# Kernel tuning notes

Measured on AMD Instinct MI355X. Metric: run time of the kernel, lower is better.

## Reference

```python
import jax, jax.numpy as jnp
import numpy as np

IN_DIM = 2048
OUT_DIM = 2048
BASIS_DIM = 64
BATCH = 4
SEQ = 4096
EPS = 1e-5


def _make_bbasis():
    k = np.arange(BASIS_DIM, dtype=np.float64)[:, None]  # (K,1)
    i = np.arange(OUT_DIM, dtype=np.float64)[None, :]    # (1,D)
    return jnp.asarray(np.cos(2.0 * np.pi * (k + 1.0) / (i + 2.0)), dtype=jnp.float32)


def setup_inputs() -> dict:
    key = jax.random.key(0)
    k1, k2, k3, k4 = jax.random.split(key, 4)
    x = jax.random.normal(k1, (BATCH, SEQ, IN_DIM), dtype=jnp.float32)
    # nn.init.uniform_(-0.1, 0.1) style scaling for weights
    W = jax.random.uniform(k2, (OUT_DIM, IN_DIM), dtype=jnp.float32, minval=-0.1, maxval=0.1)
    W_res = jax.random.uniform(k3, (OUT_DIM, IN_DIM), dtype=jnp.float32, minval=-0.1, maxval=0.1)
    Acoeff = jax.random.uniform(k4, (OUT_DIM, BASIS_DIM), dtype=jnp.float32, minval=-0.1, maxval=0.1)
    gamma = jnp.ones((OUT_DIM,), dtype=jnp.float32)
    beta = jnp.zeros((OUT_DIM,), dtype=jnp.float32)
    Bbasis = _make_bbasis()
    return {"x": x, "W": W, "W_res": W_res, "gamma": gamma, "beta": beta,
            "Acoeff": Acoeff, "Bbasis": Bbasis}


def reference(x, W, W_res, gamma, beta, Acoeff, Bbasis):
    # residual projection (use_residual == 'separate')
    residual = jnp.einsum('bsi,oi->bso', x, W_res)          # (B,S,D)
    transformed = jnp.einsum('bsi,oi->bso', x, W)           # (B,S,D)
    # LayerNorm over last dim
    mean = jnp.mean(transformed, axis=-1, keepdims=True)
    var = jnp.mean(jnp.square(transformed - mean), axis=-1, keepdims=True)
    normalized = (transformed - mean) * jax.lax.rsqrt(var + EPS) * gamma + beta
    # periodic basis gather
    seq_len = x.shape[1]
    j = jnp.arange(seq_len) % BASIS_DIM                      # (S,)
    B_vec = Bbasis[j]                                        # (S,D)
    A_vec = Acoeff[:, j].T                                   # (S,D)
    scalars = jnp.einsum('bsd,sd->bs', normalized, B_vec)    # (B,S)
    return scalars[:, :, None] * A_vec[None] + residual      # (B,S,D)
```

## Files before the change

kernel.cpp:

```cpp
#include <hip/hip_runtime.h>
#include <hip/hip_bf16.h>

#define KDIM   2048
#define DDIM   2048
#define MROWS  16384
#define BASIS  64
#define EPSLN  1e-5f

typedef __bf16 bf16x8 __attribute__((ext_vector_type(8)));
typedef float  f32x4  __attribute__((ext_vector_type(4)));

static __device__ __forceinline__ unsigned short f2bf(float f) {
  union { float f; unsigned int u; } v; v.f = f;
  unsigned int r = v.u + 0x7FFFu + ((v.u >> 16) & 1u);
  return (unsigned short)(r >> 16);
}

__global__ __launch_bounds__(256) void cast_f32_bf16(
    const float* __restrict__ in, unsigned short* __restrict__ out, int n4) {
  int i = blockIdx.x * blockDim.x + threadIdx.x;
  int stride = gridDim.x * blockDim.x;
  for (; i < n4; i += stride) {
    float4 v = ((const float4*)in)[i];
    ushort4 o;
    o.x = f2bf(v.x); o.y = f2bf(v.y); o.z = f2bf(v.z); o.w = f2bf(v.w);
    ((ushort4*)out)[i] = o;
  }
}

__global__ __launch_bounds__(256) void transpose_acoeff(
    const float* __restrict__ Ac, float* __restrict__ At) {
  int j = blockIdx.x;
  for (int d = threadIdx.x; d < DDIM; d += blockDim.x)
    At[j * DDIM + d] = Ac[d * BASIS + j];
}

__device__ __forceinline__ void gload16(const void* g, void* l) {
  __builtin_amdgcn_global_load_lds(
      (const __attribute__((address_space(1))) unsigned int*)(unsigned long long)g,
      (__attribute__((address_space(3))) unsigned int*)(unsigned int)(unsigned long long)l,
      16, 0, 0);
}

__global__ __launch_bounds__(256) void gemm_dual(
    const unsigned short* __restrict__ Abf,
    const unsigned short* __restrict__ Bbf,
    float* __restrict__ Tout,
    float* __restrict__ Rout)
{
  __shared__ __align__(16) unsigned short As[128 * 64];
  __shared__ __align__(16) unsigned short Bs[128 * 64];

  const int tid   = threadIdx.x;
  const int lane  = tid & 63;
  const int wave  = tid >> 6;
  const int bx    = blockIdx.x;
  const int by    = blockIdx.y;
  const int brow0 = by * 128;
  const int bcol0 = bx * 128;

  const int srow  = lane >> 3;
  const int sslot = (lane & 7) ^ srow;
  const unsigned short* pA = Abf + (size_t)(brow0 + wave * 8 + srow) * KDIM + sslot * 8;
  const unsigned short* pB = Bbf + (size_t)(bcol0 + wave * 8 + srow) * KDIM + sslot * 8;

  const int wm   = wave >> 1;
  const int wn   = wave & 1;
  const int frow = lane & 15;
  const int kgrp = lane >> 4;
  const int swz  = lane & 7;

  f32x4 acc[4][4] = {};

  for (int kt = 0; kt < KDIM; kt += 64) {
#pragma unroll
    for (int c = 0; c < 4; ++c) {
      gload16(pA + (size_t)c * 32 * KDIM + kt, As + c * 2048 + wave * 512);
      gload16(pB + (size_t)c * 32 * KDIM + kt, Bs + c * 2048 + wave * 512);
    }
    __syncthreads();
#pragma unroll
    for (int ko = 0; ko < 8; ko += 4) {
      bf16x8 af[4], bv[4];
#pragma unroll
      for (int i = 0; i < 4; ++i) {
        int row = wm * 64 + i * 16 + frow;
        af[i] = *(const bf16x8*)((const char*)As + row * 128 + (((ko + kgrp) ^ swz) * 16));
      }
#pragma unroll
      for (int j = 0; j < 4; ++j) {
        int row = wn * 64 + j * 16 + frow;
        bv[j] = *(const bf16x8*)((const char*)Bs + row * 128 + (((ko + kgrp) ^ swz) * 16));
      }
#pragma unroll
      for (int i = 0; i < 4; ++i)
#pragma unroll
        for (int j = 0; j < 4; ++j)
          acc[i][j] = __builtin_amdgcn_mfma_f32_16x16x32_bf16(af[i], bv[j], acc[i][j], 0, 0, 0);
    }
    __syncthreads();
  }

  float* Cb   = (bx < 16) ? Tout : Rout;
  const int c0 = (bx < 16) ? bcol0 : (bcol0 - 2048);
#pragma unroll
  for (int i = 0; i < 4; ++i) {
    const int r0 = brow0 + wm * 64 + i * 16 + kgrp * 4;
#pragma unroll
    for (int j = 0; j < 4; ++j) {
      const int col = c0 + wn * 64 + j * 16 + frow;
#pragma unroll
      for (int r = 0; r < 4; ++r)
        Cb[(size_t)(r0 + r) * DDIM + col] = acc[i][j][r];
    }
  }
}

__global__ __launch_bounds__(256) void epilogue(
    const float* __restrict__ T, const float* __restrict__ Bb,
    const float* __restrict__ At, const float* __restrict__ gam,
    const float* __restrict__ bet, float* __restrict__ out)
{
  __shared__ float red[16];
  const int row = blockIdx.x;
  const int s   = row & 4095;
  const int j   = s & 63;
  const int tid = threadIdx.x;
  const size_t rb = (size_t)row * DDIM;
  const int d0 = tid * 8;

  float4 t0 = *(const float4*)(T + rb + d0);
  float4 t1 = *(const float4*)(T + rb + d0 + 4);

  float sum = t0.x + t0.y + t0.z + t0.w + t1.x + t1.y + t1.z + t1.w;
  float sq  = t0.x*t0.x + t0.y*t0.y + t0.z*t0.z + t0.w*t0.w
            + t1.x*t1.x + t1.y*t1.y + t1.z*t1.z + t1.w*t1.w;
#pragma unroll
  for (int off = 32; off > 0; off >>= 1) {
    sum += __shfl_down(sum, off);
    sq  += __shfl_down(sq,  off);
  }
  if ((tid & 63) == 0) { red[tid >> 6] = sum; red[4 + (tid >> 6)] = sq; }
  __syncthreads();
  if (tid == 0) {
    float sAll = red[0] + red[1] + red[2] + red[3];
    float qAll = red[4] + red[5] + red[6] + red[7];
    float m = sAll * (1.0f / 2048.0f);
    float v = qAll * (1.0f / 2048.0f) - m * m;
    red[8] = m;
    red[9] = rsqrtf(v + EPSLN);
  }
  __syncthreads();
  const float mean = red[8], rstd = red[9];

  const size_t jb = (size_t)j * DDIM;
  float4 g0 = *(const float4*)(gam + d0), g1 = *(const float4*)(gam + d0 + 4);
  float4 b0 = *(const float4*)(bet + d0), b1 = *(const float4*)(bet + d0 + 4);
  float4 w0 = *(const float4*)(Bb + jb + d0), w1 = *(const float4*)(Bb + jb + d0 + 4);

  float sc =
      ((t0.x - mean) * rstd * g0.x + b0.x) * w0.x +
      ((t0.y - mean) * rstd * g0.y + b0.y) * w0.y +
      ((t0.z - mean) * rstd * g0.z + b0.z) * w0.z +
      ((t0.w - mean) * rstd * g0.w + b0.w) * w0.w +
      ((t1.x - mean) * rstd * g1.x + b1.x) * w1.x +
      ((t1.y - mean) * rstd * g1.y + b1.y) * w1.y +
      ((t1.z - mean) * rstd * g1.z + b1.z) * w1.z +
      ((t1.w - mean) * rstd * g1.w + b1.w) * w1.w;
#pragma unroll
  for (int off = 32; off > 0; off >>= 1) sc += __shfl_down(sc, off);
  if ((tid & 63) == 0) red[10 + (tid >> 6)] = sc;
  __syncthreads();
  const float scalar = red[10] + red[11] + red[12] + red[13];

  float4 a0 = *(const float4*)(At + jb + d0), a1 = *(const float4*)(At + jb + d0 + 4);
  float4 o0 = *(const float4*)(out + rb + d0), o1 = *(const float4*)(out + rb + d0 + 4);
  o0.x = scalar * a0.x + o0.x;  o0.y = scalar * a0.y + o0.y;
  o0.z = scalar * a0.z + o0.z;  o0.w = scalar * a0.w + o0.w;
  o1.x = scalar * a1.x + o1.x;  o1.y = scalar * a1.y + o1.y;
  o1.z = scalar * a1.z + o1.z;  o1.w = scalar * a1.w + o1.w;
  *(float4*)(out + rb + d0)     = o0;
  *(float4*)(out + rb + d0 + 4) = o1;
}

extern "C" void kernel_launch(void* const* d_in, const int* in_sizes, int n_in,
                              void* d_out, int out_size, void* d_ws, size_t ws_size,
                              hipStream_t stream) {
  const float* x      = (const float*)d_in[0];
  const float* W      = (const float*)d_in[1];
  const float* Wres   = (const float*)d_in[2];
  const float* gamma  = (const float*)d_in[3];
  const float* beta   = (const float*)d_in[4];
  const float* Acoeff = (const float*)d_in[5];
  const float* Bbasis = (const float*)d_in[6];
  float* out = (float*)d_out;
  char* ws = (char*)d_ws;

  unsigned short* xbf = (unsigned short*)ws;
  unsigned short* Wc  = (unsigned short*)(ws + 67108864);
  float* T            = (float*)(ws + 83886080);
  float* At           = (float*)(ws + 218103808);

  cast_f32_bf16<<<2048, 256, 0, stream>>>(x,    xbf,            8388608);
  cast_f32_bf16<<<512,  256, 0, stream>>>(W,    Wc,             1048576);
  cast_f32_bf16<<<512,  256, 0, stream>>>(Wres, Wc + 4194304,   1048576);
  transpose_acoeff<<<64, 256, 0, stream>>>(Acoeff, At);

  dim3 grid(32, 128);
  gemm_dual<<<grid, 256, 0, stream>>>(xbf, Wc, T, out);

  epilogue<<<16384, 256, 0, stream>>>(T, Bbasis, At, gamma, beta, out);
}
```

Baseline: 623.6 us.

## Use 256x256 double-buffered GEMM tiles with swizzled grid and bf16 intermediate

```diff
diff --git a/kernel.cpp b/kernel.cpp
--- a/kernel.cpp
+++ b/kernel.cpp
@@ -6,14 +6,20 @@
 #define MROWS  16384
 #define BASIS  64
 #define EPSLN  1e-5f
+#define NKT    32
 
 typedef __bf16 bf16x8 __attribute__((ext_vector_type(8)));
 typedef float  f32x4  __attribute__((ext_vector_type(4)));
+typedef unsigned short u16x8 __attribute__((ext_vector_type(8)));
 
 static __device__ __forceinline__ unsigned short f2bf(float f) {
   union { float f; unsigned int u; } v; v.f = f;
   unsigned int r = v.u + 0x7FFFu + ((v.u >> 16) & 1u);
   return (unsigned short)(r >> 16);
+}
+static __device__ __forceinline__ float bf2f(unsigned short h) {
+  union { unsigned int u; float f; } v; v.u = ((unsigned int)h) << 16;
+  return v.f;
 }
 
 __global__ __launch_bounds__(256) void cast_f32_bf16(
@@ -42,82 +48,147 @@
       16, 0, 0);
 }
 
-__global__ __launch_bounds__(256) void gemm_dual(
+__device__ __forceinline__ void bar() {
+  asm volatile("s_barrier" ::: "memory");
+}
+
+__global__ __launch_bounds__(512, 2) void gemm_dual(
     const unsigned short* __restrict__ Abf,
     const unsigned short* __restrict__ Bbf,
-    float* __restrict__ Tout,
+    unsigned short* __restrict__ Tout,
     float* __restrict__ Rout)
 {
-  __shared__ __align__(16) unsigned short As[128 * 64];
-  __shared__ __align__(16) unsigned short Bs[128 * 64];
-
-  const int tid   = threadIdx.x;
-  const int lane  = tid & 63;
-  const int wave  = tid >> 6;
-  const int bx    = blockIdx.x;
-  const int by    = blockIdx.y;
-  const int brow0 = by * 128;
-  const int bcol0 = bx * 128;
-
-  const int srow  = lane >> 3;
-  const int sslot = (lane & 7) ^ srow;
-  const unsigned short* pA = Abf + (size_t)(brow0 + wave * 8 + srow) * KDIM + sslot * 8;
-  const unsigned short* pB = Bbf + (size_t)(bcol0 + wave * 8 + srow) * KDIM + sslot * 8;
-
-  const int wm   = wave >> 1;
-  const int wn   = wave & 1;
+  __shared__ __align__(16) unsigned short As[2 * 256 * 64];
+  __shared__ __align__(16) unsigned short Bs[2 * 256 * 64];
+
+  const int tid  = threadIdx.x;
+  const int lane = tid & 63;
+  const int wave = tid >> 6;
+
+  const int bid = blockIdx.x;
+  const int wg  = (bid & 7) * 128 + (bid >> 3);
+  const int bm  = wg >> 4;
+  const int bn  = wg & 15;
+  const int brow0 = bm * 256;
+  const int bcol0 = bn * 256;
+
+  const int srow  = tid >> 3;
+  const int sslot = (tid & 7) ^ (srow & 7);
+  const unsigned short* pA = Abf + (size_t)(brow0 + srow) * KDIM + sslot * 8;
+  const unsigned short* pB = Bbf + (size_t)(bcol0 + srow) * KDIM + sslot * 8;
+  const int ldst = wave * 512;
+
+  const int wm   = wave >> 2;
+  const int wn   = wave & 3;
   const int frow = lane & 15;
   const int kgrp = lane >> 4;
-  const int swz  = lane & 7;
-
-  f32x4 acc[4][4] = {};
-
-  for (int kt = 0; kt < KDIM; kt += 64) {
-#pragma unroll
-    for (int c = 0; c < 4; ++c) {
-      gload16(pA + (size_t)c * 32 * KDIM + kt, As + c * 2048 + wave * 512);
-      gload16(pB + (size_t)c * 32 * KDIM + kt, Bs + c * 2048 + wave * 512);
-    }
-    __syncthreads();
-#pragma unroll
-    for (int ko = 0; ko < 8; ko += 4) {
-      bf16x8 af[4], bv[4];
+  const int swz  = frow & 7;
+
+  f32x4 acc[8][4] = {};
+
+#pragma unroll
+  for (int c = 0; c < 4; ++c) {
+    gload16(pA + (size_t)c * 64 * KDIM,      As + c * 4096 + ldst);
+    gload16(pB + (size_t)c * 64 * KDIM,      Bs + c * 4096 + ldst);
+  }
+#pragma unroll
+  for (int c = 0; c < 4; ++c) {
+    gload16(pA + (size_t)c * 64 * KDIM + 64, As + 16384 + c * 4096 + ldst);
+    gload16(pB + (size_t)c * 64 * KDIM + 64, Bs + 16384 + c * 4096 + ldst);
+  }
+
+  for (int kt = 0; kt < NKT; ++kt) {
+    const unsigned short* As_b = As + (kt & 1) * 16384;
+    const unsigned short* Bs_b = Bs + (kt & 1) * 16384;
+
+    if (kt < NKT - 1) { asm volatile("s_waitcnt vmcnt(8)" ::: "memory"); }
+    else              { asm volatile("s_waitcnt vmcnt(0)" ::: "memory"); }
+    __builtin_amdgcn_sched_barrier(0);
+    bar();
+
+#pragma unroll
+    for (int ko = 0; ko < 2; ++ko) {
+      bf16x8 bv[4], af[4];
+#pragma unroll
+      for (int j = 0; j < 4; ++j) {
+        const int row = wn * 64 + j * 16 + frow;
+        bv[j] = *(const bf16x8*)(Bs_b + row * 64 + (((ko * 4 + kgrp) ^ swz) << 3));
+      }
 #pragma unroll
       for (int i = 0; i < 4; ++i) {
-        int row = wm * 64 + i * 16 + frow;
-        af[i] = *(const bf16x8*)((const char*)As + row * 128 + (((ko + kgrp) ^ swz) * 16));
-      }
-#pragma unroll
-      for (int j = 0; j < 4; ++j) {
-        int row = wn * 64 + j * 16 + frow;
-        bv[j] = *(const bf16x8*)((const char*)Bs + row * 128 + (((ko + kgrp) ^ swz) * 16));
-      }
+        const int row = wm * 128 + i * 16 + frow;
+        af[i] = *(const bf16x8*)(As_b + row * 64 + (((ko * 4 + kgrp) ^ swz) << 3));
+      }
+      bar();
+      __builtin_amdgcn_s_setprio(1);
 #pragma unroll
       for (int i = 0; i < 4; ++i)
 #pragma unroll
         for (int j = 0; j < 4; ++j)
           acc[i][j] = __builtin_amdgcn_mfma_f32_16x16x32_bf16(af[i], bv[j], acc[i][j], 0, 0, 0);
-    }
-    __syncthreads();
-  }
-
-  float* Cb   = (bx < 16) ? Tout : Rout;
-  const int c0 = (bx < 16) ? bcol0 : (bcol0 - 2048);
-#pragma unroll
-  for (int i = 0; i < 4; ++i) {
-    const int r0 = brow0 + wm * 64 + i * 16 + kgrp * 4;
-#pragma unroll
-    for (int j = 0; j < 4; ++j) {
-      const int col = c0 + wn * 64 + j * 16 + frow;
-#pragma unroll
-      for (int r = 0; r < 4; ++r)
-        Cb[(size_t)(r0 + r) * DDIM + col] = acc[i][j][r];
+      __builtin_amdgcn_s_setprio(0);
+      bar();
+#pragma unroll
+      for (int i = 0; i < 4; ++i) {
+        const int row = wm * 128 + 64 + i * 16 + frow;
+        af[i] = *(const bf16x8*)(As_b + row * 64 + (((ko * 4 + kgrp) ^ swz) << 3));
+      }
+      bar();
+      __builtin_amdgcn_s_setprio(1);
+#pragma unroll
+      for (int i = 0; i < 4; ++i)
+#pragma unroll
+        for (int j = 0; j < 4; ++j)
+          acc[4 + i][j] = __builtin_amdgcn_mfma_f32_16x16x32_bf16(af[i], bv[j], acc[4 + i][j], 0, 0, 0);
+      __builtin_amdgcn_s_setprio(0);
+      bar();
+    }
+
+    if (kt + 2 < NKT) {
+      unsigned short* Ad = As + (kt & 1) * 16384;
+      unsigned short* Bd = Bs + (kt & 1) * 16384;
+      const int k64 = (kt + 2) * 64;
+#pragma unroll
+      for (int c = 0; c < 4; ++c) {
+        gload16(pA + (size_t)c * 64 * KDIM + k64, Ad + c * 4096 + ldst);
+        gload16(pB + (size_t)c * 64 * KDIM + k64, Bd + c * 4096 + ldst);
+      }
+    }
+  }
+
+  if (bn < 8) {
+    unsigned short* Cb = Tout;
+    const int c0 = bcol0;
+#pragma unroll
+    for (int i = 0; i < 8; ++i) {
+      const int r0 = brow0 + wm * 128 + i * 16 + kgrp * 4;
+#pragma unroll
+      for (int j = 0; j < 4; ++j) {
+        const int col = c0 + wn * 64 + j * 16 + frow;
+#pragma unroll
+        for (int r = 0; r < 4; ++r)
+          Cb[(size_t)(r0 + r) * DDIM + col] = f2bf(acc[i][j][r]);
+      }
+    }
+  } else {
+    float* Cb = Rout;
+    const int c0 = bcol0 - 2048;
+#pragma unroll
+    for (int i = 0; i < 8; ++i) {
+      const int r0 = brow0 + wm * 128 + i * 16 + kgrp * 4;
+#pragma unroll
+      for (int j = 0; j < 4; ++j) {
+        const int col = c0 + wn * 64 + j * 16 + frow;
+#pragma unroll
+        for (int r = 0; r < 4; ++r)
+          Cb[(size_t)(r0 + r) * DDIM + col] = acc[i][j][r];
+      }
     }
   }
 }
 
 __global__ __launch_bounds__(256) void epilogue(
-    const float* __restrict__ T, const float* __restrict__ Bb,
+    const unsigned short* __restrict__ T, const float* __restrict__ Bb,
     const float* __restrict__ At, const float* __restrict__ gam,
     const float* __restrict__ bet, float* __restrict__ out)
 {
@@ -129,12 +200,14 @@
   const size_t rb = (size_t)row * DDIM;
   const int d0 = tid * 8;
 
-  float4 t0 = *(const float4*)(T + rb + d0);
-  float4 t1 = *(const float4*)(T + rb + d0 + 4);
-
-  float sum = t0.x + t0.y + t0.z + t0.w + t1.x + t1.y + t1.z + t1.w;
-  float sq  = t0.x*t0.x + t0.y*t0.y + t0.z*t0.z + t0.w*t0.w
-            + t1.x*t1.x + t1.y*t1.y + t1.z*t1.z + t1.w*t1.w;
+  u16x8 tv = *(const u16x8*)(T + rb + d0);
+  float t[8];
+#pragma unroll
+  for (int k = 0; k < 8; ++k) t[k] = bf2f(tv[k]);
+
+  float sum = 0.f, sq = 0.f;
+#pragma unroll
+  for (int k = 0; k < 8; ++k) { sum += t[k]; sq += t[k] * t[k]; }
 #pragma unroll
   for (int off = 32; off > 0; off >>= 1) {
     sum += __shfl_down(sum, off);
@@ -159,14 +232,14 @@
   float4 w0 = *(const float4*)(Bb + jb + d0), w1 = *(const float4*)(Bb + jb + d0 + 4);
 
   float sc =
-      ((t0.x - mean) * rstd * g0.x + b0.x) * w0.x +
-      ((t0.y - mean) * rstd * g0.y + b0.y) * w0.y +
-      ((t0.z - mean) * rstd * g0.z + b0.z) * w0.z +
-      ((t0.w - mean) * rstd * g0.w + b0.w) * w0.w +
-      ((t1.x - mean) * rstd * g1.x + b1.x) * w1.x +
-      ((t1.y - mean) * rstd * g1.y + b1.y) * w1.y +
-      ((t1.z - mean) * rstd * g1.z + b1.z) * w1.z +
-      ((t1.w - mean) * rstd * g1.w + b1.w) * w1.w;
+      ((t[0] - mean) * rstd * g0.x + b0.x) * w0.x +
+      ((t[1] - mean) * rstd * g0.y + b0.y) * w0.y +
+      ((t[2] - mean) * rstd * g0.z + b0.z) * w0.z +
+      ((t[3] - mean) * rstd * g0.w + b0.w) * w0.w +
+      ((t[4] - mean) * rstd * g1.x + b1.x) * w1.x +
+      ((t[5] - mean) * rstd * g1.y + b1.y) * w1.y +
+      ((t[6] - mean) * rstd * g1.z + b1.z) * w1.z +
+      ((t[7] - mean) * rstd * g1.w + b1.w) * w1.w;
 #pragma unroll
   for (int off = 32; off > 0; off >>= 1) sc += __shfl_down(sc, off);
   if ((tid & 63) == 0) red[10 + (tid >> 6)] = sc;
@@ -198,16 +271,15 @@
 
   unsigned short* xbf = (unsigned short*)ws;
   unsigned short* Wc  = (unsigned short*)(ws + 67108864);
-  float* T            = (float*)(ws + 83886080);
-  float* At           = (float*)(ws + 218103808);
+  unsigned short* T   = (unsigned short*)(ws + 83886080);
+  float* At           = (float*)(ws + 150994944);
 
   cast_f32_bf16<<<2048, 256, 0, stream>>>(x,    xbf,            8388608);
   cast_f32_bf16<<<512,  256, 0, stream>>>(W,    Wc,             1048576);
   cast_f32_bf16<<<512,  256, 0, stream>>>(Wres, Wc + 4194304,   1048576);
   transpose_acoeff<<<64, 256, 0, stream>>>(Acoeff, At);
 
-  dim3 grid(32, 128);
-  gemm_dual<<<grid, 256, 0, stream>>>(xbf, Wc, T, out);
+  gemm_dual<<<1024, 512, 0, stream>>>(xbf, Wc, T, out);
 
   epilogue<<<16384, 256, 0, stream>>>(T, Bbasis, At, gamma, beta, out);
 }
```

Result: no change. 612.2 us (-1.8%).
